# Kernel optimization log

Measured on AMD Instinct MI355X. Metric: run time of the kernel, lower is better.

The kernel has to match this reference:

```python
import jax, jax.numpy as jnp
import numpy as np

EPSILON = 1e-8

def setup_inputs() -> dict:
    key = jax.random.key(0)
    k1, k2, k3, k4 = jax.random.split(key, 4)
    B, C_in, C_out, H, W, S, K = 16, 512, 512, 32, 32, 512, 3
    x = jax.random.normal(k1, (B, C_in, H, W), dtype=jnp.float32)
    w = jax.random.normal(k2, (B, S), dtype=jnp.float32)
    # Linear(style_dim -> in_chan), bias initialized to ones per module code
    style_w = jax.random.normal(k3, (C_in, S), dtype=jnp.float32) * (1.0 / np.sqrt(S))
    style_b = jnp.ones((C_in,), dtype=jnp.float32)
    # kaiming_normal_(fan_in, leaky_relu): std = sqrt(2/(1+0.01^2)) / sqrt(fan_in)
    fan_in = C_in * K * K
    gain = np.sqrt(2.0 / (1.0 + 0.01 ** 2))
    weight = jax.random.normal(k4, (C_out, C_in, K, K), dtype=jnp.float32) * (gain / np.sqrt(fan_in))
    return {"x": x, "w": w, "style_w": style_w, "style_b": style_b, "weight": weight}

def reference(x, w, style_w, style_b, weight):
    B, C, H, W_ = x.shape
    C_out, _, K, _ = weight.shape
    # style modulation: Linear(style_dim -> in_chan)
    style = w @ style_w.T + style_b                       # (B, C_in)
    weights = style[:, None, :, None, None] * weight[None]  # (B, C_out, C_in, K, K)
    # demodulation
    d = jax.lax.rsqrt(jnp.sum(weights * weights, axis=(2, 3, 4), keepdims=True) + EPSILON)
    weights = weights * d
    # grouped conv with groups = batch
    pad = 1 if K > 1 else 0
    xg = x.reshape(1, B * C, H, W_)
    wg = weights.reshape(B * C_out, C, K, K)
    y = jax.lax.conv_general_dilated(
        xg, wg, window_strides=(1, 1), padding=((pad, pad), (pad, pad)),
        dimension_numbers=("NCHW", "OIHW", "NCHW"), feature_group_count=B)
    return y.reshape(B, C_out, H, W_)
```

## Files before the change

### kernel.cpp

```cpp
#include <hip/hip_runtime.h>
#include <hip/hip_bf16.h>

#define NB 16
#define CI 512
#define CO 512
#define HW 1024
#define SD 512
#define EPSI 1e-8f

typedef __attribute__((ext_vector_type(8))) short bf16x8;
typedef __attribute__((ext_vector_type(16))) float f32x16;
typedef __attribute__((ext_vector_type(4))) unsigned int u32x4;

#define GLOAD_LDS16(g, l) __builtin_amdgcn_global_load_lds( \
    (const __attribute__((address_space(1))) unsigned int*)(const void*)(g), \
    (__attribute__((address_space(3))) unsigned int*)(void*)(l), 16, 0, 0)
#define SCHED0() __builtin_amdgcn_sched_barrier(0)
#define SBAR()   __builtin_amdgcn_s_barrier()

__global__ void k_style2(const float* __restrict__ w, const float* __restrict__ sw,
                         const float* __restrict__ sb, float* __restrict__ style) {
    int gw = (blockIdx.x * 256 + threadIdx.x) >> 6;
    int l = threadIdx.x & 63;
    int b = gw >> 9, c = gw & 511;
    const float4* wr = (const float4*)(w + b * SD) + (l << 1);
    const float4* sr = (const float4*)(sw + c * SD) + (l << 1);
    float4 a0 = wr[0], a1 = wr[1], q0 = sr[0], q1 = sr[1];
    float acc = a0.x * q0.x + a0.y * q0.y + a0.z * q0.z + a0.w * q0.w
              + a1.x * q1.x + a1.y * q1.y + a1.z * q1.z + a1.w * q1.w;
#pragma unroll
    for (int off = 32; off > 0; off >>= 1) acc += __shfl_down(acc, off);
    if (l == 0) style[gw] = acc + sb[c];
}

__global__ void k_wprep(const float* __restrict__ wt, float* __restrict__ wsq,
                        __hip_bfloat16* __restrict__ wtb) {
    int idx = blockIdx.x * 256 + threadIdx.x;
    const float* p = wt + idx * 9;
    float a = 0.f;
#pragma unroll
    for (int t = 0; t < 9; ++t) {
        float v = p[t];
        a += v * v;
        wtb[t * (CO * CI) + idx] = __float2bfloat16(v);
    }
    wsq[idx] = a;
}

__global__ void k_demod2(const float* __restrict__ style, const float* __restrict__ wsq,
                         float* __restrict__ dv) {
    int gw = (blockIdx.x * 256 + threadIdx.x) >> 6;
    int l = threadIdx.x & 63;
    int b = gw >> 9, co = gw & 511;
    const float4* st = (const float4*)(style + b * CI) + (l << 1);
    const float4* wq = (const float4*)(wsq + co * CI) + (l << 1);
    float4 s0 = st[0], s1 = st[1], q0 = wq[0], q1 = wq[1];
    float acc = s0.x * s0.x * q0.x + s0.y * s0.y * q0.y + s0.z * s0.z * q0.z + s0.w * s0.w * q0.w
              + s1.x * s1.x * q1.x + s1.y * s1.y * q1.y + s1.z * s1.z * q1.z + s1.w * s1.w * q1.w;
#pragma unroll
    for (int off = 32; off > 0; off >>= 1) acc += __shfl_down(acc, off);
    if (l == 0) dv[gw] = rsqrtf(acc + EPSI);
}

__global__ void k_xs(const float* __restrict__ x, const float* __restrict__ style,
                     __hip_bfloat16* __restrict__ xs) {
    __shared__ float tile[32][33];
    int b = blockIdx.z, c0 = blockIdx.y * 32, p0 = blockIdx.x * 32;
    int tx = threadIdx.x & 31, ty = threadIdx.x >> 5;
#pragma unroll
    for (int i = 0; i < 4; ++i) {
        int ci = c0 + ty + i * 8;
        tile[ty + i * 8][tx] = x[(b * CI + ci) * HW + p0 + tx] * style[b * CI + ci];
    }
    __syncthreads();
#pragma unroll
    for (int i = 0; i < 4; ++i) {
        int p = p0 + ty + i * 8;
        xs[(b * HW + p) * CI + c0 + tx] = __float2bfloat16(tile[tx][ty + i * 8]);
    }
}

#define XS_BYTES 52224
#define WBUF_BYTES 16384
#define SMEM_TOTAL (2 * XS_BYTES + 3 * WBUF_BYTES)

extern "C" __global__ __launch_bounds__(256, 1) void k_conv(
        const __hip_bfloat16* __restrict__ wtb,
        const __hip_bfloat16* __restrict__ xs,
        const float* __restrict__ dvec,
        float* __restrict__ out) {
    extern __shared__ char smem[];
    char* Xs  = smem;
    char* Wsb = smem + 2 * XS_BYTES;

    const int tid  = threadIdx.x;
    const int lane = tid & 63;
    const int wv   = tid >> 6;
    const int wn   = wv & 1;
    const int wb   = wv >> 1;

    int bid = blockIdx.x;
    int xcd = bid & 7, idx = bid >> 3;
    int cot = xcd >> 1;
    int px8 = idx & 7;
    int bp  = (idx >> 3) | ((xcd & 1) << 2);
    const int co0 = cot * 128;
    const int p0  = px8 * 128;
    const int y0  = px8 * 4;
    const int b0  = bp * 2;
    const int b   = b0 + wb;
    const bool xedge = (px8 == 0) || (px8 == 7);

    if (tid < 192) {
        int g = tid & 7;
        int rx = ((tid >> 3) & 1) ? 33 : 0;
        int row = tid >> 4;
        int off = (row * 34 + rx) * 128 + g * 16;
        *(u32x4*)(Xs + off) = (u32x4){0, 0, 0, 0};
        *(u32x4*)(Xs + XS_BYTES + off) = (u32x4){0, 0, 0, 0};
    }

    const int srcgW = (lane & 7) ^ (lane >> 3);

    auto issueW = [&](int tap, int cin, int bufi) {
        const __hip_bfloat16* wsrc = wtb + ((size_t)tap * CO + co0) * CI + cin;
        char* wdst = Wsb + bufi * WBUF_BYTES;
#pragma unroll
        for (int k = 0; k < 4; ++k) {
            int seg = k * 4 + wv;
            int co_l = seg * 8 + (lane >> 3);
            GLOAD_LDS16(wsrc + co_l * CI + srcgW * 8, wdst + seg * 1024);
        }
    };
    auto issueX = (void*)nullptr; (void)issueX;

    f32x16 acc[4][2];
#pragma unroll
    for (int m = 0; m < 4; ++m)
#pragma unroll
        for (int n = 0; n < 2; ++n)
            acc[m][n] = (f32x16)(0.f);

    issueW(0, 0, 0);
    issueW(1, 0, 1);
    {
        char* Xdst = Xs;
#pragma unroll
        for (int k = 0; k < 12; ++k) {
            int sid = k * 4 + wv;
            int bb = (k >= 6) ? 1 : 0;
            int rem = sid - bb * 24;
            int ry = rem >> 2, seg = rem & 3;
            int rx0 = 1 + seg * 8;
            char* ldst = Xdst + ((bb * 6 + ry) * 34 + rx0) * 128;
            int y = y0 - 1 + ry;
            int rx = rx0 + (lane >> 3);
            int srcg = (lane & 7) ^ (rx & 7);
            if ((unsigned)y < 32u)
                GLOAD_LDS16(xs + ((size_t)(b0 + bb) * HW + (y << 5) + (rx - 1)) * CI + 0 + srcg * 8, ldst);
            else
                *(u32x4*)(ldst + (lane << 4)) = (u32x4){0, 0, 0, 0};
        }
    }
    SCHED0();
    asm volatile("s_waitcnt lgkmcnt(0) vmcnt(0)" ::: "memory");
    SCHED0();
    SBAR();
    SCHED0();

    for (int cc = 0; cc < 8; ++cc) {
        const char* Xcur = Xs + (cc & 1) * XS_BYTES;
#pragma unroll
        for (int t = 0; t < 9; ++t) {
            if (!(cc == 7 && t >= 7)) {
                const int tn  = (t <= 6) ? (t + 2) : (t - 7);
                const int cin = ((t <= 6) ? cc : (cc + 1)) * 64;
                issueW(tn, cin, (t + 2) % 3);
            }
            if (t == 0 && cc < 7) {
                char* Xdst = Xs + ((cc + 1) & 1) * XS_BYTES;
                const int cin = (cc + 1) * 64;
#pragma unroll
                for (int k = 0; k < 12; ++k) {
                    int sid = k * 4 + wv;
                    int bb = (k >= 6) ? 1 : 0;
                    int rem = sid - bb * 24;
                    int ry = rem >> 2, seg = rem & 3;
                    int rx0 = 1 + seg * 8;
                    char* ldst = Xdst + ((bb * 6 + ry) * 34 + rx0) * 128;
                    int y = y0 - 1 + ry;
                    int rx = rx0 + (lane >> 3);
                    int srcg = (lane & 7) ^ (rx & 7);
                    if ((unsigned)y < 32u)
                        GLOAD_LDS16(xs + ((size_t)(b0 + bb) * HW + (y << 5) + (rx - 1)) * CI + cin + srcg * 8, ldst);
                    else
                        *(u32x4*)(ldst + (lane << 4)) = (u32x4){0, 0, 0, 0};
                }
            }
            SCHED0();

            const char* Wb = Wsb + (t % 3) * WBUF_BYTES;
            const int ky = t / 3, kx = t - (t / 3) * 3;
#pragma unroll
            for (int q = 0; q < 4; ++q) {
                bf16x8 afr[4], bfr[2];
                int g = (q << 1) + (lane >> 5);
#pragma unroll
                for (int m = 0; m < 4; ++m)
                    afr[m] = *(const bf16x8*)(Wb + (m * 32 + (lane & 31)) * 128 +
                                              ((g ^ (lane & 7)) << 4));
#pragma unroll
                for (int n = 0; n < 2; ++n) {
                    int ry = wn * 2 + n + ky;
                    int rx = (lane & 31) + kx;
                    bfr[n] = *(const bf16x8*)(Xcur + ((wb * 6 + ry) * 34 + rx) * 128 +
                                              ((g ^ (rx & 7)) << 4));
                }
#pragma unroll
                for (int m = 0; m < 4; ++m)
#pragma unroll
                    for (int n = 0; n < 2; ++n)
                        acc[m][n] = __builtin_amdgcn_mfma_f32_32x32x16_bf16(afr[m], bfr[n], acc[m][n], 0, 0, 0);
            }

            if (!(cc == 7 && t == 8)) {
                SCHED0();
                if (cc < 7 && t < 2) {
                    if (xedge) asm volatile("s_waitcnt lgkmcnt(0) vmcnt(14)" ::: "memory");
                    else       asm volatile("s_waitcnt lgkmcnt(0) vmcnt(16)" ::: "memory");
                } else if (cc == 7 && t == 7) {
                    asm volatile("s_waitcnt lgkmcnt(0) vmcnt(0)" ::: "memory");
                } else {
                    asm volatile("s_waitcnt lgkmcnt(0) vmcnt(4)" ::: "memory");
                }
                SCHED0();
                SBAR();
                SCHED0();
            }
        }
    }

#pragma unroll
    for (int m = 0; m < 4; ++m) {
#pragma unroll
        for (int r = 0; r < 16; ++r) {
            int co = co0 + m * 32 + (r & 3) + ((r >> 2) << 3) + ((lane >> 5) << 2);
            float dvv = dvec[b * CO + co];
            float* orow = out + ((size_t)b * CO + co) * HW + p0 + wn * 64;
            orow[lane & 31]        = acc[m][0][r] * dvv;
            orow[32 + (lane & 31)] = acc[m][1][r] * dvv;
        }
    }
}

extern "C" void kernel_launch(void* const* d_in, const int* in_sizes, int n_in,
                              void* d_out, int out_size, void* d_ws, size_t ws_size,
                              hipStream_t stream) {
    const float* x  = (const float*)d_in[0];
    const float* w  = (const float*)d_in[1];
    const float* sw = (const float*)d_in[2];
    const float* sb = (const float*)d_in[3];
    const float* wt = (const float*)d_in[4];
    float* out = (float*)d_out;

    char* ws = (char*)d_ws;
    float* style = (float*)(ws);
    float* dvec  = (float*)(ws + 32768);
    float* wsq   = (float*)(ws + 65536);
    __hip_bfloat16* wtb = (__hip_bfloat16*)(ws + 1114112);
    __hip_bfloat16* xsb = (__hip_bfloat16*)(ws + 5832704);

    hipFuncSetAttribute((const void*)k_conv,
                        hipFuncAttributeMaxDynamicSharedMemorySize, SMEM_TOTAL);

    k_style2<<<2048, 256, 0, stream>>>(w, sw, sb, style);
    k_wprep<<<1024, 256, 0, stream>>>(wt, wsq, wtb);
    k_xs<<<dim3(32, 16, 16), 256, 0, stream>>>(x, style, xsb);
    k_demod2<<<2048, 256, 0, stream>>>(style, wsq, dvec);
    k_conv<<<256, 256, SMEM_TOTAL, stream>>>(wtb, xsb, dvec, out);
}
```

Before: 97.69 us.

## Split conv block across eight waves and use a zero page for padding loads

The conv kernel now runs 512 threads per block instead of 256. Each wave computes a 64-channel half of the output tile, so its accumulators drop to 2x2 and it issues half as many weight and input loads. Out-of-range padding rows are loaded asynchronously from a zeroed global page rather than written to shared memory directly. This makes every wave's load count uniform, so the edge-specific vmcnt waits go away, and MFMA sections are wrapped in s_setprio. More waves can hide latency better, but shared-memory fragment reads per MFMA go up and register use per wave changes.

```diff
diff --git a/kernel.cpp b/kernel.cpp
--- a/kernel.cpp
+++ b/kernel.cpp
@@ -34,7 +34,9 @@
 }
 
 __global__ void k_wprep(const float* __restrict__ wt, float* __restrict__ wsq,
-                        __hip_bfloat16* __restrict__ wtb) {
+                        __hip_bfloat16* __restrict__ wtb, u32x4* __restrict__ zpage) {
+    if (blockIdx.x == 0 && threadIdx.x < 64)
+        zpage[threadIdx.x] = (u32x4){0, 0, 0, 0};
     int idx = blockIdx.x * 256 + threadIdx.x;
     const float* p = wt + idx * 9;
     float a = 0.f;
@@ -84,10 +86,11 @@
 #define WBUF_BYTES 16384
 #define SMEM_TOTAL (2 * XS_BYTES + 3 * WBUF_BYTES)
 
-extern "C" __global__ __launch_bounds__(256, 1) void k_conv(
+extern "C" __global__ __launch_bounds__(512, 2) void k_conv(
         const __hip_bfloat16* __restrict__ wtb,
         const __hip_bfloat16* __restrict__ xs,
         const float* __restrict__ dvec,
+        const char* __restrict__ zpage,
         float* __restrict__ out) {
     extern __shared__ char smem[];
     char* Xs  = smem;
@@ -96,8 +99,9 @@
     const int tid  = threadIdx.x;
     const int lane = tid & 63;
     const int wv   = tid >> 6;
+    const int wb   = wv >> 2;
+    const int wr   = (wv >> 1) & 1;
     const int wn   = wv & 1;
-    const int wb   = wv >> 1;
 
     int bid = blockIdx.x;
     int xcd = bid & 7, idx = bid >> 3;
@@ -109,7 +113,6 @@
     const int y0  = px8 * 4;
     const int b0  = bp * 2;
     const int b   = b0 + wb;
-    const bool xedge = (px8 == 0) || (px8 == 7);
 
     if (tid < 192) {
         int g = tid & 7;
@@ -126,29 +129,17 @@
         const __hip_bfloat16* wsrc = wtb + ((size_t)tap * CO + co0) * CI + cin;
         char* wdst = Wsb + bufi * WBUF_BYTES;
 #pragma unroll
-        for (int k = 0; k < 4; ++k) {
-            int seg = k * 4 + wv;
+        for (int k = 0; k < 2; ++k) {
+            int seg = k * 8 + wv;
             int co_l = seg * 8 + (lane >> 3);
             GLOAD_LDS16(wsrc + co_l * CI + srcgW * 8, wdst + seg * 1024);
         }
     };
-    auto issueX = (void*)nullptr; (void)issueX;
-
-    f32x16 acc[4][2];
-#pragma unroll
-    for (int m = 0; m < 4; ++m)
-#pragma unroll
-        for (int n = 0; n < 2; ++n)
-            acc[m][n] = (f32x16)(0.f);
-
-    issueW(0, 0, 0);
-    issueW(1, 0, 1);
-    {
-        char* Xdst = Xs;
-#pragma unroll
-        for (int k = 0; k < 12; ++k) {
-            int sid = k * 4 + wv;
-            int bb = (k >= 6) ? 1 : 0;
+    auto issueX = [&](char* Xdst, int cin) {
+#pragma unroll
+        for (int k = 0; k < 6; ++k) {
+            int sid = k * 8 + wv;
+            int bb = (sid >= 24) ? 1 : 0;
             int rem = sid - bb * 24;
             int ry = rem >> 2, seg = rem & 3;
             int rx0 = 1 + seg * 8;
@@ -157,11 +148,22 @@
             int rx = rx0 + (lane >> 3);
             int srcg = (lane & 7) ^ (rx & 7);
             if ((unsigned)y < 32u)
-                GLOAD_LDS16(xs + ((size_t)(b0 + bb) * HW + (y << 5) + (rx - 1)) * CI + 0 + srcg * 8, ldst);
+                GLOAD_LDS16(xs + ((size_t)(b0 + bb) * HW + (y << 5) + (rx - 1)) * CI + cin + srcg * 8, ldst);
             else
-                *(u32x4*)(ldst + (lane << 4)) = (u32x4){0, 0, 0, 0};
-        }
-    }
+                GLOAD_LDS16(zpage, ldst);
+        }
+    };
+
+    f32x16 acc[2][2];
+#pragma unroll
+    for (int m = 0; m < 2; ++m)
+#pragma unroll
+        for (int n = 0; n < 2; ++n)
+            acc[m][n] = (f32x16)(0.f);
+
+    issueW(0, 0, 0);
+    issueW(1, 0, 1);
+    issueX(Xs, 0);
     SCHED0();
     asm volatile("s_waitcnt lgkmcnt(0) vmcnt(0)" ::: "memory");
     SCHED0();
@@ -177,38 +179,22 @@
                 const int cin = ((t <= 6) ? cc : (cc + 1)) * 64;
                 issueW(tn, cin, (t + 2) % 3);
             }
-            if (t == 0 && cc < 7) {
-                char* Xdst = Xs + ((cc + 1) & 1) * XS_BYTES;
-                const int cin = (cc + 1) * 64;
-#pragma unroll
-                for (int k = 0; k < 12; ++k) {
-                    int sid = k * 4 + wv;
-                    int bb = (k >= 6) ? 1 : 0;
-                    int rem = sid - bb * 24;
-                    int ry = rem >> 2, seg = rem & 3;
-                    int rx0 = 1 + seg * 8;
-                    char* ldst = Xdst + ((bb * 6 + ry) * 34 + rx0) * 128;
-                    int y = y0 - 1 + ry;
-                    int rx = rx0 + (lane >> 3);
-                    int srcg = (lane & 7) ^ (rx & 7);
-                    if ((unsigned)y < 32u)
-                        GLOAD_LDS16(xs + ((size_t)(b0 + bb) * HW + (y << 5) + (rx - 1)) * CI + cin + srcg * 8, ldst);
-                    else
-                        *(u32x4*)(ldst + (lane << 4)) = (u32x4){0, 0, 0, 0};
-                }
-            }
+            if (t == 0 && cc < 7)
+                issueX(Xs + ((cc + 1) & 1) * XS_BYTES, (cc + 1) * 64);
             SCHED0();
 
             const char* Wb = Wsb + (t % 3) * WBUF_BYTES;
             const int ky = t / 3, kx = t - (t / 3) * 3;
+            __builtin_amdgcn_s_setprio(1);
 #pragma unroll
             for (int q = 0; q < 4; ++q) {
-                bf16x8 afr[4], bfr[2];
+                bf16x8 afr[2], bfr[2];
                 int g = (q << 1) + (lane >> 5);
 #pragma unroll
-                for (int m = 0; m < 4; ++m)
-                    afr[m] = *(const bf16x8*)(Wb + (m * 32 + (lane & 31)) * 128 +
-                                              ((g ^ (lane & 7)) << 4));
+                for (int m = 0; m < 2; ++m) {
+                    int cr = wr * 64 + m * 32 + (lane & 31);
+                    afr[m] = *(const bf16x8*)(Wb + cr * 128 + ((g ^ (cr & 7)) << 4));
+                }
 #pragma unroll
                 for (int n = 0; n < 2; ++n) {
                     int ry = wn * 2 + n + ky;
@@ -217,22 +203,21 @@
                                               ((g ^ (rx & 7)) << 4));
                 }
 #pragma unroll
-                for (int m = 0; m < 4; ++m)
+                for (int m = 0; m < 2; ++m)
 #pragma unroll
                     for (int n = 0; n < 2; ++n)
                         acc[m][n] = __builtin_amdgcn_mfma_f32_32x32x16_bf16(afr[m], bfr[n], acc[m][n], 0, 0, 0);
             }
+            __builtin_amdgcn_s_setprio(0);
 
             if (!(cc == 7 && t == 8)) {
                 SCHED0();
-                if (cc < 7 && t < 2) {
-                    if (xedge) asm volatile("s_waitcnt lgkmcnt(0) vmcnt(14)" ::: "memory");
-                    else       asm volatile("s_waitcnt lgkmcnt(0) vmcnt(16)" ::: "memory");
-                } else if (cc == 7 && t == 7) {
+                if (cc < 7 && t < 2)
+                    asm volatile("s_waitcnt lgkmcnt(0) vmcnt(8)" ::: "memory");
+                else if (cc == 7 && t == 7)
                     asm volatile("s_waitcnt lgkmcnt(0) vmcnt(0)" ::: "memory");
-                } else {
-                    asm volatile("s_waitcnt lgkmcnt(0) vmcnt(4)" ::: "memory");
-                }
+                else
+                    asm volatile("s_waitcnt lgkmcnt(0) vmcnt(2)" ::: "memory");
                 SCHED0();
                 SBAR();
                 SCHED0();
@@ -241,10 +226,10 @@
     }
 
 #pragma unroll
-    for (int m = 0; m < 4; ++m) {
+    for (int m = 0; m < 2; ++m) {
 #pragma unroll
         for (int r = 0; r < 16; ++r) {
-            int co = co0 + m * 32 + (r & 3) + ((r >> 2) << 3) + ((lane >> 5) << 2);
+            int co = co0 + wr * 64 + m * 32 + (r & 3) + ((r >> 2) << 3) + ((lane >> 5) << 2);
             float dvv = dvec[b * CO + co];
             float* orow = out + ((size_t)b * CO + co) * HW + p0 + wn * 64;
             orow[lane & 31]        = acc[m][0][r] * dvv;
@@ -269,13 +254,14 @@
     float* wsq   = (float*)(ws + 65536);
     __hip_bfloat16* wtb = (__hip_bfloat16*)(ws + 1114112);
     __hip_bfloat16* xsb = (__hip_bfloat16*)(ws + 5832704);
+    char* zpage = ws + 22609920;
 
     hipFuncSetAttribute((const void*)k_conv,
                         hipFuncAttributeMaxDynamicSharedMemorySize, SMEM_TOTAL);
 
     k_style2<<<2048, 256, 0, stream>>>(w, sw, sb, style);
-    k_wprep<<<1024, 256, 0, stream>>>(wt, wsq, wtb);
+    k_wprep<<<1024, 256, 0, stream>>>(wt, wsq, (__hip_bfloat16*)wtb, (u32x4*)zpage);
     k_xs<<<dim3(32, 16, 16), 256, 0, stream>>>(x, style, xsb);
     k_demod2<<<2048, 256, 0, stream>>>(style, wsq, dvec);
-    k_conv<<<256, 256, SMEM_TOTAL, stream>>>(wtb, xsb, dvec, out);
-}
+    k_conv<<<256, 512, SMEM_TOTAL, stream>>>(wtb, xsb, dvec, zpage, out);
+}
```

Result: faster. 95.00 us (-2.8%).
